# Kernel optimization log

Measured on AMD Instinct MI355X. Metric: run time of the kernel, lower is better.

The kernel has to match this reference:

```python
import jax, jax.numpy as jnp
import numpy as np


def _maxpool2x2(t):
    # t: [B, H, W, C] -> [B, H//2, W//2, C], 2x2 max pool stride 2
    B, H, W, C = t.shape
    return t.reshape(B, H // 2, 2, W // 2, 2, C).max(axis=(2, 4))


def setup_inputs() -> dict:
    key = jax.random.key(0)
    ks = jax.random.split(key, 7)
    B, H, W, C = 16, 64, 64, 256
    x = jax.random.normal(ks[0], (B, H, W, C), jnp.float32)
    w_theta = jax.random.normal(ks[1], (C, C // 8), jnp.float32) * 0.05
    w_phi = jax.random.normal(ks[2], (C, C // 8), jnp.float32) * 0.05
    w_g = jax.random.normal(ks[3], (C, C // 2), jnp.float32) * 0.05
    w_o = jax.random.normal(ks[4], (C // 2, C), jnp.float32) * 0.05
    b_o = jnp.zeros((C,), jnp.float32)
    sigma = jax.random.normal(ks[5], (), jnp.float32)
    return {"x": x, "w_theta": w_theta, "w_phi": w_phi, "w_g": w_g,
            "w_o": w_o, "b_o": b_o, "sigma": sigma}


def reference(x, w_theta, w_phi, w_g, w_o, b_o, sigma):
    B, H, W, C = x.shape
    L = H * W          # location_num = 4096
    Ld = L // 4        # downsampled_num (after 2x2 maxpool)
    # 1x1 convs == channel GEMMs
    theta = jnp.einsum('bhwc,cd->bhwd', x, w_theta).reshape(B, L, C // 8)
    phi = jnp.einsum('bhwc,cd->bhwd', x, w_phi)
    phi = _maxpool2x2(phi).reshape(B, Ld, C // 8)
    attn = jax.nn.softmax(jnp.einsum('bld,bmd->blm', theta, phi), axis=-1)  # [B, L, Ld]
    g = jnp.einsum('bhwc,cd->bhwd', x, w_g)
    g = _maxpool2x2(g).reshape(B, Ld, C // 2)
    attn_g = jnp.einsum('blm,bmd->bld', attn, g).reshape(B, H, W, C // 2)
    attn_g = jnp.einsum('bhwd,dc->bhwc', attn_g, w_o) + b_o
    return x + sigma * attn_g
```

## Files before the change

### kernel.cpp

```cpp
#include <hip/hip_runtime.h>
#include <hip/hip_bf16.h>


typedef __attribute__((ext_vector_type(8))) short bf16x8;
typedef __attribute__((ext_vector_type(4))) float f32x4;

#define MFMA16(A,B,C) __builtin_amdgcn_mfma_f32_16x16x32_bf16(A,B,C,0,0,0)

#define GLOAD16(GSRC, LDST)                                                        \
    __builtin_amdgcn_global_load_lds(                                              \
        (const __attribute__((address_space(1))) unsigned int*)(GSRC),             \
        (__attribute__((address_space(3))) unsigned int*)(LDST), 16, 0, 0)

static __device__ __forceinline__ unsigned short f2b(float f) {
    __hip_bfloat16 h = __float2bfloat16(f);
    return *reinterpret_cast<unsigned short*>(&h);
}
static __device__ __forceinline__ unsigned short bmax(unsigned short a, unsigned short b) {
    return (__uint_as_float((unsigned)a << 16) > __uint_as_float((unsigned)b << 16)) ? a : b;
}
static __device__ __forceinline__ float fexp2(float f) {
    return __builtin_amdgcn_exp2f(f);
}

__global__ void k_prep(const float* __restrict__ w_theta, const float* __restrict__ w_phi,
                       const float* __restrict__ w_g, const float* __restrict__ w_o,
                       unsigned short* __restrict__ WT, unsigned short* __restrict__ woT)
{
    int bid = blockIdx.x, t = threadIdx.x;
    if (bid < 192) {
        int n = bid;
        float v;
        if (n < 32)      v = w_theta[t * 32 + n] * 1.44269504f;
        else if (n < 64) v = w_phi[t * 32 + (n - 32)];
        else             v = w_g[t * 128 + (n - 64)];
        WT[n * 256 + t] = f2b(v);
    } else if (t < 128) {
        int cc = bid - 192;
        woT[cc * 128 + t] = f2b(w_o[t * 256 + cc]);
    }
}

__global__ __launch_bounds__(256) void k_proj(
    const float* __restrict__ x, const unsigned short* __restrict__ WT,
    unsigned short* __restrict__ theta_b, unsigned short* __restrict__ phi_p,
    unsigned short* __restrict__ g_pT)
{
    __shared__ char plds[40960];
    unsigned short* xT = (unsigned short*)plds;
    unsigned short* wT = (unsigned short*)(plds + 16384);

    const int t = threadIdx.x;
    const int w = t >> 6, l = t & 63, G = l >> 4, c = l & 15;
    const int bid = blockIdx.x;
    const int b = bid >> 5, h2 = bid & 31;
    const size_t row0 = (size_t)bid * 128;

    f32x4 acc[2][12];
#pragma unroll
    for (int i = 0; i < 2; i++)
#pragma unroll
        for (int j = 0; j < 12; j++) acc[i][j] = (f32x4){0.f, 0.f, 0.f, 0.f};

    for (int k0 = 0; k0 < 256; k0 += 64) {
        __syncthreads();
#pragma unroll
        for (int it = 0; it < 4; it++) {
            int u = it * 256 + t, r = u >> 3, s = u & 7;
            const float* px = x + (row0 + r) * 256 + k0 + s * 8;
            float4 a = *(const float4*)px;
            float4 bq = *(const float4*)(px + 4);
            uint4 v;
            v.x = (unsigned)f2b(a.x) | ((unsigned)f2b(a.y) << 16);
            v.y = (unsigned)f2b(a.z) | ((unsigned)f2b(a.w) << 16);
            v.z = (unsigned)f2b(bq.x) | ((unsigned)f2b(bq.y) << 16);
            v.w = (unsigned)f2b(bq.z) | ((unsigned)f2b(bq.w) << 16);
            *(uint4*)((char*)xT + r * 128 + ((s * 16) ^ ((r & 7) << 4))) = v;
        }
#pragma unroll
        for (int it = 0; it < 6; it++) {
            int u = it * 256 + t, r = u >> 3, s = u & 7;
            uint4 v = *(const uint4*)(WT + r * 256 + k0 + s * 8);
            *(uint4*)((char*)wT + r * 128 + ((s * 16) ^ ((r & 7) << 4))) = v;
        }
        __syncthreads();
#pragma unroll
        for (int kin = 0; kin < 2; kin++) {
            int m0r = (2 * w) * 16 + c, m1r = (2 * w + 1) * 16 + c;
            bf16x8 a0 = *(const bf16x8*)((char*)xT + m0r * 128 + ((kin * 64 + G * 16) ^ ((m0r & 7) << 4)));
            bf16x8 a1 = *(const bf16x8*)((char*)xT + m1r * 128 + ((kin * 64 + G * 16) ^ ((m1r & 7) << 4)));
#pragma unroll
            for (int nt = 0; nt < 12; nt++) {
                int nr = nt * 16 + c;
                bf16x8 bv = *(const bf16x8*)((char*)wT + nr * 128 + ((kin * 64 + G * 16) ^ ((nr & 7) << 4)));
                acc[0][nt] = MFMA16(a0, bv, acc[0][nt]);
                acc[1][nt] = MFMA16(a1, bv, acc[1][nt]);
            }
        }
    }

#pragma unroll
    for (int mt = 0; mt < 2; mt++)
#pragma unroll
        for (int nt = 0; nt < 2; nt++)
#pragma unroll
            for (int i = 0; i < 4; i++) {
                size_t row = row0 + (2 * w + mt) * 16 + 4 * G + i;
                theta_b[row * 32 + nt * 16 + c] = f2b(acc[mt][nt][i]);
            }

    __syncthreads();

#pragma unroll
    for (int mt = 0; mt < 2; mt++) {
        int rl = 2 * w + mt, rr = rl >> 2, wpb = (rl & 3) * 8 + 2 * G;
#pragma unroll
        for (int nt = 2; nt < 12; nt++) {
            int col = (nt - 2) * 16 + c;
#pragma unroll
            for (int j = 0; j < 2; j++) {
                int row = rr * 32 + wpb + j;
                float m = fmaxf(acc[mt][nt][2 * j], acc[mt][nt][2 * j + 1]);
                *(unsigned short*)(plds + row * 512 + ((2 * col) ^ ((row & 7) << 4))) = f2b(m);
            }
        }
    }
    __syncthreads();

    {
        int wp = t >> 3, chb = (t & 7) * 4;
        unsigned short vv[4];
#pragma unroll
        for (int k = 0; k < 4; k++) {
            int colb = 2 * (chb + k);
            unsigned short a = *(const unsigned short*)(plds + wp * 512 + (colb ^ ((wp & 7) << 4)));
            unsigned short e = *(const unsigned short*)(plds + (wp + 32) * 512 + (colb ^ ((wp & 7) << 4)));
            vv[k] = bmax(a, e);
        }
        uint2 pv;
        pv.x = (unsigned)vv[0] | ((unsigned)vv[1] << 16);
        pv.y = (unsigned)vv[2] | ((unsigned)vv[3] << 16);
        *(uint2*)(phi_p + ((size_t)(b * 1024 + h2 * 32 + wp)) * 32 + chb) = pv;
    }
#pragma unroll
    for (int it = 0; it < 2; it++) {
        int d = t & 127, s4 = (t >> 7) + 2 * it;
        union { unsigned short v[8]; uint4 q; } pk;
#pragma unroll
        for (int k = 0; k < 8; k++) {
            int wp2 = 16 * (k >> 2) + 4 * s4 + (k & 3);
            int colb = 2 * (32 + d);
            unsigned short a = *(const unsigned short*)(plds + wp2 * 512 + (colb ^ ((wp2 & 7) << 4)));
            unsigned short e = *(const unsigned short*)(plds + (wp2 + 32) * 512 + (colb ^ ((wp2 & 7) << 4)));
            pk.v[k] = bmax(a, e);
        }
        *(uint4*)(g_pT + ((size_t)b * 128 + d) * 1024 + h2 * 32 + s4 * 8) = pk.q;
    }
}

__global__ __launch_bounds__(256, 4) void k_attn(
    const unsigned short* __restrict__ theta_b, const unsigned short* __restrict__ phi_p,
    const unsigned short* __restrict__ g_pT, const unsigned short* __restrict__ woT,
    const float* __restrict__ x, const float* __restrict__ b_o,
    const float* __restrict__ sigma_p, float* __restrict__ out)
{
    __shared__ char lds[40960];

    const int t = threadIdx.x;
    const int w = t >> 6, l = t & 63, G = l >> 4, c = l & 15;
    const int qg = w >> 1, mg = w & 1;
    const int bid = (blockIdx.x & 7) * 128 + (blockIdx.x >> 3);
    const int b = bid >> 6;
    const int q0 = (bid & 63) * 64;
    const int xr = (c & 7) << 4;

    const unsigned short* gsrc = g_pT + (size_t)b * 131072;
    const unsigned short* psrc = phi_p + (size_t)b * 32768;
#define STAGE(BI, MC)                                                               \
    {                                                                               \
        char* gb = lds + mg * 20480 + (BI) * 10240;                                 \
        char* pb = gb + 8192;                                                       \
        const int hp = mg * 16 + (MC);                                              \
        _Pragma("unroll")                                                           \
        for (int it = 0; it < 4; it++) {                                            \
            int d = 64 * qg + 16 * it + (l >> 2);                                   \
            GLOAD16(gsrc + (size_t)d * 1024 + hp * 32 + (l & 3) * 8,                \
                    gb + qg * 4096 + it * 1024 + l * 16);                           \
        }                                                                           \
        {                                                                           \
            int r = 16 * qg + (l >> 2);                                             \
            GLOAD16(psrc + (size_t)(hp * 32 + r) * 32 + (l & 3) * 8,                \
                    pb + qg * 1024 + l * 16);                                       \
        }                                                                           \
    }

    STAGE(0, 0);
    {
        char* th = lds + 10240;
        int r = t >> 2, s = t & 3;
        uint4 v = *(const uint4*)(theta_b + ((size_t)(b * 4096 + q0 + r)) * 32 + s * 8);
        *(uint4*)(th + r * 64 + s * 16) = v;
    }
    __syncthreads();

    const bf16x8 bt0 = *(const bf16x8*)(lds + 10240 + (qg * 32 + c) * 64 + G * 16);
    const bf16x8 bt1 = *(const bf16x8*)(lds + 10240 + (qg * 32 + 16 + c) * 64 + G * 16);
    __syncthreads();

    f32x4 oacc[2][8];
#pragma unroll
    for (int qt = 0; qt < 2; qt++)
#pragma unroll
        for (int dt = 0; dt < 8; dt++) oacc[qt][dt] = (f32x4){0.f, 0.f, 0.f, 0.f};
    float ps[2] = {0.f, 0.f};
    const f32x4 zf = (f32x4){0.f, 0.f, 0.f, 0.f};

    for (int mc = 0; mc < 16; mc++) {
        const int cur = mc & 1;
        asm volatile("s_waitcnt vmcnt(0)" ::: "memory");
        __builtin_amdgcn_sched_barrier(0);
        __builtin_amdgcn_s_barrier();
        __builtin_amdgcn_sched_barrier(0);
        if (mc < 15) STAGE(cur ^ 1, mc + 1);

        const char* gL   = lds + mg * 20480 + cur * 10240;
        const char* phiL = gL + 8192;

        bf16x8 ap0 = *(const bf16x8*)(phiL + c * 64 + G * 16);
        bf16x8 ap1 = *(const bf16x8*)(phiL + (16 + c) * 64 + G * 16);
        f32x4 sacc[2][2];
        __builtin_amdgcn_s_setprio(1);
        sacc[0][0] = MFMA16(ap0, bt0, zf);
        sacc[0][1] = MFMA16(ap1, bt0, zf);
        sacc[1][0] = MFMA16(ap0, bt1, zf);
        sacc[1][1] = MFMA16(ap1, bt1, zf);
        __builtin_amdgcn_s_setprio(0);

        bf16x8 pa[2];
#pragma unroll
        for (int qt = 0; qt < 2; qt++) {
            union { unsigned u[4]; bf16x8 v; } pu;
#pragma unroll
            for (int mt = 0; mt < 2; mt++)
#pragma unroll
                for (int hf = 0; hf < 2; hf++) {
                    float p0 = fexp2(sacc[qt][mt][2 * hf]);
                    float p1 = fexp2(sacc[qt][mt][2 * hf + 1]);
                    ps[qt] += p0 + p1;
                    pu.u[mt * 2 + hf] = (unsigned)f2b(p0) | ((unsigned)f2b(p1) << 16);
                }
            pa[qt] = pu.v;
        }

        __builtin_amdgcn_s_setprio(1);
#pragma unroll
        for (int dt = 0; dt < 8; dt++) {
            bf16x8 bg = *(const bf16x8*)(gL + (dt * 16 + c) * 64 + G * 16);
            oacc[0][dt] = MFMA16(pa[0], bg, oacc[0][dt]);
            oacc[1][dt] = MFMA16(pa[1], bg, oacc[1][dt]);
        }
        __builtin_amdgcn_s_setprio(0);
    }
#undef STAGE
    __syncthreads();

#pragma unroll
    for (int qt = 0; qt < 2; qt++) {
        ps[qt] += __shfl_xor(ps[qt], 16);
        ps[qt] += __shfl_xor(ps[qt], 32);
    }

    if (mg == 1) {
        char* po = lds + qg * 16640;
#pragma unroll
        for (int qt = 0; qt < 2; qt++)
#pragma unroll
            for (int dt = 0; dt < 8; dt++)
#pragma unroll
                for (int i = 0; i < 4; i++)
                    *(float*)(po + (qt * 16 + 4 * G + i) * 520 + (dt * 16 + c) * 4) =
                        oacc[qt][dt][i];
        if (l < 16) {
            *(float*)(lds + 33280 + (qg * 32 + l) * 4)      = ps[0];
            *(float*)(lds + 33280 + (qg * 32 + 16 + l) * 4) = ps[1];
        }
    }
    __syncthreads();
    if (mg == 0) {
        const char* po = lds + qg * 16640;
#pragma unroll
        for (int qt = 0; qt < 2; qt++)
#pragma unroll
            for (int dt = 0; dt < 8; dt++) {
                f32x4 a = oacc[qt][dt];
#pragma unroll
                for (int i = 0; i < 4; i++)
                    a[i] += *(const float*)(po + (qt * 16 + 4 * G + i) * 520 + (dt * 16 + c) * 4);
                oacc[qt][dt] = a;
            }
#pragma unroll
        for (int qt = 0; qt < 2; qt++)
            ps[qt] += *(const float*)(lds + 33280 + (qg * 32 + qt * 16 + c) * 4);
        float rinv[2][4];
#pragma unroll
        for (int qt = 0; qt < 2; qt++)
#pragma unroll
            for (int i = 0; i < 4; i++)
                rinv[qt][i] = 1.0f / __shfl(ps[qt], 4 * G + i);
        char* Or = lds + qg * 16640;
#pragma unroll
        for (int qt = 0; qt < 2; qt++)
#pragma unroll
            for (int dt = 0; dt < 8; dt++)
#pragma unroll
                for (int i = 0; i < 4; i++) {
                    int r32 = qt * 16 + 4 * G + i, d = dt * 16 + c;
                    *(unsigned short*)(Or + r32 * 256 + ((d * 2) ^ ((r32 & 7) << 4))) =
                        f2b(oacc[qt][dt][i] * rinv[qt][i]);
                }
    }
    __syncthreads();

    const float sg = *sigma_p;
    const char* O_r = lds + (w >> 1) * 16640 + ((w & 1) * 16 + c) * 256;
    char* wo_l = lds + 8448;
    bf16x8 aO[4];
#pragma unroll
    for (int ks = 0; ks < 4; ks++)
        aO[ks] = *(const bf16x8*)(O_r + ((ks * 64 + G * 16) ^ xr));

    for (int cb = 0; cb < 8; cb++) {
        __syncthreads();
#pragma unroll
        for (int it = 0; it < 2; it++) {
            int u = it * 256 + t, r = u >> 4, s = u & 15;
            uint4 v = *(const uint4*)(woT + (size_t)(cb * 32 + r) * 128 + s * 8);
            *(uint4*)(wo_l + r * 256 + ((s * 16) ^ ((r & 7) << 4))) = v;
        }
        __syncthreads();
        f32x4 eacc[2];
#pragma unroll
        for (int ct = 0; ct < 2; ct++) eacc[ct] = (f32x4){0.f, 0.f, 0.f, 0.f};
#pragma unroll
        for (int ks = 0; ks < 4; ks++) {
#pragma unroll
            for (int ct = 0; ct < 2; ct++) {
                bf16x8 bw = *(const bf16x8*)(wo_l + (ct * 16 + c) * 256 + ((ks * 64 + G * 16) ^ xr));
                eacc[ct] = MFMA16(aO[ks], bw, eacc[ct]);
            }
        }
#pragma unroll
        for (int ct = 0; ct < 2; ct++) {
            int col = cb * 32 + ct * 16 + c;
            float bo = b_o[col];
#pragma unroll
            for (int i = 0; i < 4; i++) {
                size_t off = ((size_t)(b * 4096 + q0 + w * 16 + 4 * G + i)) * 256 + col;
                out[off] = x[off] + sg * (eacc[ct][i] + bo);
            }
        }
    }
}

extern "C" void kernel_launch(void* const* d_in, const int* in_sizes, int n_in,
                              void* d_out, int out_size, void* d_ws, size_t ws_size,
                              hipStream_t stream)
{
    const float* x       = (const float*)d_in[0];
    const float* w_theta = (const float*)d_in[1];
    const float* w_phi   = (const float*)d_in[2];
    const float* w_g     = (const float*)d_in[3];
    const float* w_o     = (const float*)d_in[4];
    const float* b_o     = (const float*)d_in[5];
    const float* sigma   = (const float*)d_in[6];
    float* out = (float*)d_out;

    char* ws = (char*)d_ws;
    unsigned short* theta_b = (unsigned short*)(ws);
    unsigned short* phi_p   = (unsigned short*)(ws + 4194304);
    unsigned short* g_pT    = (unsigned short*)(ws + 5242880);
    unsigned short* WT      = (unsigned short*)(ws + 9437184);
    unsigned short* woT     = (unsigned short*)(ws + 9535488);

    hipLaunchKernelGGL(k_prep, dim3(448), dim3(256), 0, stream,
                       w_theta, w_phi, w_g, w_o, WT, woT);
    hipLaunchKernelGGL(k_proj, dim3(512), dim3(256), 0, stream,
                       x, WT, theta_b, phi_p, g_pT);
    hipLaunchKernelGGL(k_attn, dim3(1024), dim3(256), 0, stream,
                       theta_b, phi_p, g_pT, woT, x, b_o, sigma, out);
}
```

Before: 69.76 us.

## Double attention block to 512 threads, one 16-row query tile per wave

```diff
diff --git a/kernel.cpp b/kernel.cpp
--- a/kernel.cpp
+++ b/kernel.cpp
@@ -158,7 +158,7 @@
     }
 }
 
-__global__ __launch_bounds__(256, 4) void k_attn(
+__global__ __launch_bounds__(512, 8) void k_attn(
     const unsigned short* __restrict__ theta_b, const unsigned short* __restrict__ phi_p,
     const unsigned short* __restrict__ g_pT, const unsigned short* __restrict__ woT,
     const float* __restrict__ x, const float* __restrict__ b_o,
@@ -182,13 +182,13 @@
         char* pb = gb + 8192;                                                       \
         const int hp = mg * 16 + (MC);                                              \
         _Pragma("unroll")                                                           \
-        for (int it = 0; it < 4; it++) {                                            \
-            int d = 64 * qg + 16 * it + (l >> 2);                                   \
+        for (int it = 0; it < 2; it++) {                                            \
+            int d = qg * 32 + it * 16 + (l >> 2);                                   \
             GLOAD16(gsrc + (size_t)d * 1024 + hp * 32 + (l & 3) * 8,                \
-                    gb + qg * 4096 + it * 1024 + l * 16);                           \
+                    gb + qg * 2048 + it * 1024 + l * 16);                           \
         }                                                                           \
-        {                                                                           \
-            int r = 16 * qg + (l >> 2);                                             \
+        if (qg < 2) {                                                               \
+            int r = qg * 16 + (l >> 2);                                             \
             GLOAD16(psrc + (size_t)(hp * 32 + r) * 32 + (l & 3) * 8,                \
                     pb + qg * 1024 + l * 16);                                       \
         }                                                                           \
@@ -197,22 +197,19 @@
     STAGE(0, 0);
     {
         char* th = lds + 10240;
-        int r = t >> 2, s = t & 3;
-        uint4 v = *(const uint4*)(theta_b + ((size_t)(b * 4096 + q0 + r)) * 32 + s * 8);
-        *(uint4*)(th + r * 64 + s * 16) = v;
-    }
-    __syncthreads();
-
-    const bf16x8 bt0 = *(const bf16x8*)(lds + 10240 + (qg * 32 + c) * 64 + G * 16);
-    const bf16x8 bt1 = *(const bf16x8*)(lds + 10240 + (qg * 32 + 16 + c) * 64 + G * 16);
-    __syncthreads();
-
-    f32x4 oacc[2][8];
-#pragma unroll
-    for (int qt = 0; qt < 2; qt++)
-#pragma unroll
-        for (int dt = 0; dt < 8; dt++) oacc[qt][dt] = (f32x4){0.f, 0.f, 0.f, 0.f};
-    float ps[2] = {0.f, 0.f};
+        int r = t >> 3, s = t & 7;
+        uint2 v = *(const uint2*)(theta_b + ((size_t)(b * 4096 + q0 + r)) * 32 + s * 4);
+        *(uint2*)(th + r * 64 + s * 8) = v;
+    }
+    __syncthreads();
+
+    const bf16x8 bt = *(const bf16x8*)(lds + 10240 + (qg * 16 + c) * 64 + G * 16);
+    __syncthreads();
+
+    f32x4 oacc[8];
+#pragma unroll
+    for (int dt = 0; dt < 8; dt++) oacc[dt] = (f32x4){0.f, 0.f, 0.f, 0.f};
+    float ps = 0.f;
     const f32x4 zf = (f32x4){0.f, 0.f, 0.f, 0.f};
 
     for (int mc = 0; mc < 16; mc++) {
@@ -228,114 +225,97 @@
 
         bf16x8 ap0 = *(const bf16x8*)(phiL + c * 64 + G * 16);
         bf16x8 ap1 = *(const bf16x8*)(phiL + (16 + c) * 64 + G * 16);
-        f32x4 sacc[2][2];
+        f32x4 sacc[2];
         __builtin_amdgcn_s_setprio(1);
-        sacc[0][0] = MFMA16(ap0, bt0, zf);
-        sacc[0][1] = MFMA16(ap1, bt0, zf);
-        sacc[1][0] = MFMA16(ap0, bt1, zf);
-        sacc[1][1] = MFMA16(ap1, bt1, zf);
+        sacc[0] = MFMA16(ap0, bt, zf);
+        sacc[1] = MFMA16(ap1, bt, zf);
         __builtin_amdgcn_s_setprio(0);
 
-        bf16x8 pa[2];
-#pragma unroll
-        for (int qt = 0; qt < 2; qt++) {
+        bf16x8 pa;
+        {
             union { unsigned u[4]; bf16x8 v; } pu;
 #pragma unroll
             for (int mt = 0; mt < 2; mt++)
 #pragma unroll
                 for (int hf = 0; hf < 2; hf++) {
-                    float p0 = fexp2(sacc[qt][mt][2 * hf]);
-                    float p1 = fexp2(sacc[qt][mt][2 * hf + 1]);
-                    ps[qt] += p0 + p1;
+                    float p0 = fexp2(sacc[mt][2 * hf]);
+                    float p1 = fexp2(sacc[mt][2 * hf + 1]);
+                    ps += p0 + p1;
                     pu.u[mt * 2 + hf] = (unsigned)f2b(p0) | ((unsigned)f2b(p1) << 16);
                 }
-            pa[qt] = pu.v;
+            pa = pu.v;
         }
 
         __builtin_amdgcn_s_setprio(1);
 #pragma unroll
         for (int dt = 0; dt < 8; dt++) {
             bf16x8 bg = *(const bf16x8*)(gL + (dt * 16 + c) * 64 + G * 16);
-            oacc[0][dt] = MFMA16(pa[0], bg, oacc[0][dt]);
-            oacc[1][dt] = MFMA16(pa[1], bg, oacc[1][dt]);
+            oacc[dt] = MFMA16(pa, bg, oacc[dt]);
         }
         __builtin_amdgcn_s_setprio(0);
     }
 #undef STAGE
     __syncthreads();
 
-#pragma unroll
-    for (int qt = 0; qt < 2; qt++) {
-        ps[qt] += __shfl_xor(ps[qt], 16);
-        ps[qt] += __shfl_xor(ps[qt], 32);
-    }
+    ps += __shfl_xor(ps, 16);
+    ps += __shfl_xor(ps, 32);
 
     if (mg == 1) {
-        char* po = lds + qg * 16640;
-#pragma unroll
-        for (int qt = 0; qt < 2; qt++)
-#pragma unroll
-            for (int dt = 0; dt < 8; dt++)
-#pragma unroll
-                for (int i = 0; i < 4; i++)
-                    *(float*)(po + (qt * 16 + 4 * G + i) * 520 + (dt * 16 + c) * 4) =
-                        oacc[qt][dt][i];
-        if (l < 16) {
-            *(float*)(lds + 33280 + (qg * 32 + l) * 4)      = ps[0];
-            *(float*)(lds + 33280 + (qg * 32 + 16 + l) * 4) = ps[1];
-        }
-    }
-    __syncthreads();
+        char* po = lds + qg * 8320;
+#pragma unroll
+        for (int dt = 0; dt < 8; dt++)
+#pragma unroll
+            for (int i = 0; i < 4; i++)
+                *(float*)(po + (4 * G + i) * 520 + (dt * 16 + c) * 4) = oacc[dt][i];
+        if (l < 16)
+            *(float*)(lds + 33280 + (qg * 16 + l) * 4) = ps;
+    }
+    __syncthreads();
+    float rinv[4];
     if (mg == 0) {
-        const char* po = lds + qg * 16640;
-#pragma unroll
-        for (int qt = 0; qt < 2; qt++)
-#pragma unroll
-            for (int dt = 0; dt < 8; dt++) {
-                f32x4 a = oacc[qt][dt];
-#pragma unroll
-                for (int i = 0; i < 4; i++)
-                    a[i] += *(const float*)(po + (qt * 16 + 4 * G + i) * 520 + (dt * 16 + c) * 4);
-                oacc[qt][dt] = a;
-            }
-#pragma unroll
-        for (int qt = 0; qt < 2; qt++)
-            ps[qt] += *(const float*)(lds + 33280 + (qg * 32 + qt * 16 + c) * 4);
-        float rinv[2][4];
-#pragma unroll
-        for (int qt = 0; qt < 2; qt++)
+        const char* po = lds + qg * 8320;
+#pragma unroll
+        for (int dt = 0; dt < 8; dt++) {
+            f32x4 a = oacc[dt];
 #pragma unroll
             for (int i = 0; i < 4; i++)
-                rinv[qt][i] = 1.0f / __shfl(ps[qt], 4 * G + i);
-        char* Or = lds + qg * 16640;
-#pragma unroll
-        for (int qt = 0; qt < 2; qt++)
-#pragma unroll
-            for (int dt = 0; dt < 8; dt++)
-#pragma unroll
-                for (int i = 0; i < 4; i++) {
-                    int r32 = qt * 16 + 4 * G + i, d = dt * 16 + c;
-                    *(unsigned short*)(Or + r32 * 256 + ((d * 2) ^ ((r32 & 7) << 4))) =
-                        f2b(oacc[qt][dt][i] * rinv[qt][i]);
-                }
+                a[i] += *(const float*)(po + (4 * G + i) * 520 + (dt * 16 + c) * 4);
+            oacc[dt] = a;
+        }
+        ps += *(const float*)(lds + 33280 + (qg * 16 + c) * 4);
+#pragma unroll
+        for (int i = 0; i < 4; i++) rinv[i] = 1.0f / __shfl(ps, 4 * G + i);
+    }
+    __syncthreads();
+    if (mg == 0) {
+#pragma unroll
+        for (int dt = 0; dt < 8; dt++)
+#pragma unroll
+            for (int i = 0; i < 4; i++) {
+                int row = qg * 16 + 4 * G + i, d = dt * 16 + c;
+                *(unsigned short*)(lds + row * 256 + ((d * 2) ^ ((row & 7) << 4))) =
+                    f2b(oacc[dt][i] * rinv[i]);
+            }
     }
     __syncthreads();
 
     const float sg = *sigma_p;
-    const char* O_r = lds + (w >> 1) * 16640 + ((w & 1) * 16 + c) * 256;
-    char* wo_l = lds + 8448;
+    const int wq = w & 3, h = w >> 2;
+    const char* O_r = lds + (wq * 16 + c) * 256;
+    char* wo_h = lds + 16384 + h * 8192;
     bf16x8 aO[4];
 #pragma unroll
     for (int ks = 0; ks < 4; ks++)
         aO[ks] = *(const bf16x8*)(O_r + ((ks * 64 + G * 16) ^ xr));
 
-    for (int cb = 0; cb < 8; cb++) {
+    const int th256 = wq * 64 + l;
+    for (int cb = 0; cb < 4; cb++) {
         __syncthreads();
 #pragma unroll
         for (int it = 0; it < 2; it++) {
-            int u = it * 256 + t, r = u >> 4, s = u & 15;
-            uint4 v = *(const uint4*)(woT + (size_t)(cb * 32 + r) * 128 + s * 8);
-            *(uint4*)(wo_l + r * 256 + ((s * 16) ^ ((r & 7) << 4))) = v;
+            int u = it * 256 + th256, r = u >> 4, s = u & 15;
+            uint4 v = *(const uint4*)(woT + (size_t)(h * 128 + cb * 32 + r) * 128 + s * 8);
+            *(uint4*)(wo_h + r * 256 + ((s * 16) ^ ((r & 7) << 4))) = v;
         }
         __syncthreads();
         f32x4 eacc[2];
@@ -345,17 +325,17 @@
         for (int ks = 0; ks < 4; ks++) {
 #pragma unroll
             for (int ct = 0; ct < 2; ct++) {
-                bf16x8 bw = *(const bf16x8*)(wo_l + (ct * 16 + c) * 256 + ((ks * 64 + G * 16) ^ xr));
+                bf16x8 bw = *(const bf16x8*)(wo_h + (ct * 16 + c) * 256 + ((ks * 64 + G * 16) ^ xr));
                 eacc[ct] = MFMA16(aO[ks], bw, eacc[ct]);
             }
         }
 #pragma unroll
         for (int ct = 0; ct < 2; ct++) {
-            int col = cb * 32 + ct * 16 + c;
+            int col = h * 128 + cb * 32 + ct * 16 + c;
             float bo = b_o[col];
 #pragma unroll
             for (int i = 0; i < 4; i++) {
-                size_t off = ((size_t)(b * 4096 + q0 + w * 16 + 4 * G + i)) * 256 + col;
+                size_t off = ((size_t)(b * 4096 + q0 + wq * 16 + 4 * G + i)) * 256 + col;
                 out[off] = x[off] + sg * (eacc[ct][i] + bo);
             }
         }
@@ -386,6 +366,6 @@
                        w_theta, w_phi, w_g, w_o, WT, woT);
     hipLaunchKernelGGL(k_proj, dim3(512), dim3(256), 0, stream,
                        x, WT, theta_b, phi_p, g_pT);
-    hipLaunchKernelGGL(k_attn, dim3(1024), dim3(256), 0, stream,
+    hipLaunchKernelGGL(k_attn, dim3(1024), dim3(512), 0, stream,
                        theta_b, phi_p, g_pT, woT, x, b_o, sigma, out);
 }
```

Result: slower. 213.1 us (+205.5%).

## Load phi operands directly to registers, shrink LDS, use packed bf16 convert

Applied to the files above, without the earlier changes.

```diff
diff --git a/kernel.cpp b/kernel.cpp
--- a/kernel.cpp
+++ b/kernel.cpp
@@ -21,6 +21,11 @@
 }
 static __device__ __forceinline__ float fexp2(float f) {
     return __builtin_amdgcn_exp2f(f);
+}
+static __device__ __forceinline__ unsigned cvt_pk_bf16(float lo, float hi) {
+    unsigned r;
+    asm("v_cvt_pk_bf16_f32 %0, %1, %2" : "=v"(r) : "v"(lo), "v"(hi));
+    return r;
 }
 
 __global__ void k_prep(const float* __restrict__ w_theta, const float* __restrict__ w_phi,
@@ -164,7 +169,7 @@
     const float* __restrict__ x, const float* __restrict__ b_o,
     const float* __restrict__ sigma_p, float* __restrict__ out)
 {
-    __shared__ char lds[40960];
+    __shared__ char lds[36864];
 
     const int t = threadIdx.x;
     const int w = t >> 6, l = t & 63, G = l >> 4, c = l & 15;
@@ -178,8 +183,7 @@
     const unsigned short* psrc = phi_p + (size_t)b * 32768;
 #define STAGE(BI, MC)                                                               \
     {                                                                               \
-        char* gb = lds + mg * 20480 + (BI) * 10240;                                 \
-        char* pb = gb + 8192;                                                       \
+        char* gb = lds + mg * 16384 + (BI) * 8192;                                  \
         const int hp = mg * 16 + (MC);                                              \
         _Pragma("unroll")                                                           \
         for (int it = 0; it < 4; it++) {                                            \
@@ -187,25 +191,22 @@
             GLOAD16(gsrc + (size_t)d * 1024 + hp * 32 + (l & 3) * 8,                \
                     gb + qg * 4096 + it * 1024 + l * 16);                           \
         }                                                                           \
-        {                                                                           \
-            int r = 16 * qg + (l >> 2);                                             \
-            GLOAD16(psrc + (size_t)(hp * 32 + r) * 32 + (l & 3) * 8,                \
-                    pb + qg * 1024 + l * 16);                                       \
-        }                                                                           \
-    }
+    }
+#define PHI_ADDR(HP, MT) (psrc + (size_t)((HP) * 32 + (MT) * 16 + c) * 32 + G * 8)
 
     STAGE(0, 0);
+    uint4 rphi0 = *(const uint4*)PHI_ADDR(mg * 16, 0);
+    uint4 rphi1 = *(const uint4*)PHI_ADDR(mg * 16, 1);
     {
-        char* th = lds + 10240;
+        char* th = lds + 32768;
         int r = t >> 2, s = t & 3;
         uint4 v = *(const uint4*)(theta_b + ((size_t)(b * 4096 + q0 + r)) * 32 + s * 8);
         *(uint4*)(th + r * 64 + s * 16) = v;
     }
     __syncthreads();
 
-    const bf16x8 bt0 = *(const bf16x8*)(lds + 10240 + (qg * 32 + c) * 64 + G * 16);
-    const bf16x8 bt1 = *(const bf16x8*)(lds + 10240 + (qg * 32 + 16 + c) * 64 + G * 16);
-    __syncthreads();
+    const bf16x8 bt0 = *(const bf16x8*)(lds + 32768 + (qg * 32 + c) * 64 + G * 16);
+    const bf16x8 bt1 = *(const bf16x8*)(lds + 32768 + (qg * 32 + 16 + c) * 64 + G * 16);
 
     f32x4 oacc[2][8];
 #pragma unroll
@@ -223,18 +224,23 @@
         __builtin_amdgcn_sched_barrier(0);
         if (mc < 15) STAGE(cur ^ 1, mc + 1);
 
-        const char* gL   = lds + mg * 20480 + cur * 10240;
-        const char* phiL = gL + 8192;
-
-        bf16x8 ap0 = *(const bf16x8*)(phiL + c * 64 + G * 16);
-        bf16x8 ap1 = *(const bf16x8*)(phiL + (16 + c) * 64 + G * 16);
+        const char* gL = lds + mg * 16384 + cur * 8192;
+
+        bf16x8 ap0, ap1;
+        {
+            union { uint4 q; bf16x8 v; } u0, u1;
+            u0.q = rphi0; u1.q = rphi1;
+            ap0 = u0.v; ap1 = u1.v;
+        }
+        if (mc < 15) {
+            rphi0 = *(const uint4*)PHI_ADDR(mg * 16 + mc + 1, 0);
+            rphi1 = *(const uint4*)PHI_ADDR(mg * 16 + mc + 1, 1);
+        }
         f32x4 sacc[2][2];
-        __builtin_amdgcn_s_setprio(1);
         sacc[0][0] = MFMA16(ap0, bt0, zf);
         sacc[0][1] = MFMA16(ap1, bt0, zf);
         sacc[1][0] = MFMA16(ap0, bt1, zf);
         sacc[1][1] = MFMA16(ap1, bt1, zf);
-        __builtin_amdgcn_s_setprio(0);
 
         bf16x8 pa[2];
 #pragma unroll
@@ -247,21 +253,20 @@
                     float p0 = fexp2(sacc[qt][mt][2 * hf]);
                     float p1 = fexp2(sacc[qt][mt][2 * hf + 1]);
                     ps[qt] += p0 + p1;
-                    pu.u[mt * 2 + hf] = (unsigned)f2b(p0) | ((unsigned)f2b(p1) << 16);
+                    pu.u[mt * 2 + hf] = cvt_pk_bf16(p0, p1);
                 }
             pa[qt] = pu.v;
         }
 
-        __builtin_amdgcn_s_setprio(1);
 #pragma unroll
         for (int dt = 0; dt < 8; dt++) {
             bf16x8 bg = *(const bf16x8*)(gL + (dt * 16 + c) * 64 + G * 16);
             oacc[0][dt] = MFMA16(pa[0], bg, oacc[0][dt]);
             oacc[1][dt] = MFMA16(pa[1], bg, oacc[1][dt]);
         }
-        __builtin_amdgcn_s_setprio(0);
     }
 #undef STAGE
+#undef PHI_ADDR
     __syncthreads();
 
 #pragma unroll
```

Measured after the change: 71.70 us. 1.03x slower.
